# Optimization experiments

Hardware: AMD Instinct MI355X
Metric: run time of the kernel (lower is better)

## Reference

```python
import jax, jax.numpy as jnp
import numpy as np

N, F_IN, H, C, E = 50000, 128, 4, 32, 800000
NEG_SLOPE = 0.2


def setup_inputs() -> dict:
    key = jax.random.key(0)
    ks = jax.random.split(key, 6)
    x = jax.random.normal(ks[0], (N, F_IN), dtype=jnp.float32)
    edge_index = jax.random.randint(ks[1], (2, E), 0, N, dtype=jnp.int64)
    scale = 1.0 / np.sqrt(F_IN)
    Wl = jax.random.normal(ks[2], (F_IN, H * C), dtype=jnp.float32) * scale
    Wr = jax.random.normal(ks[3], (F_IN, H * C), dtype=jnp.float32) * scale
    att = jax.random.normal(ks[4], (H, C), dtype=jnp.float32) * (1.0 / np.sqrt(C))
    bias = jax.random.normal(ks[5], (H * C,), dtype=jnp.float32) * 0.01
    return {"x": x, "edge_index": edge_index, "Wl": Wl, "Wr": Wr, "att": att, "bias": bias}


def reference(x, edge_index, Wl, Wr, att, bias):
    n = x.shape[0]
    # add self loops (add_self_loops=True, edge_dim=None)
    loop = jnp.arange(n, dtype=edge_index.dtype)
    ei = jnp.concatenate([edge_index, jnp.stack([loop, loop])], axis=1)
    src, dst = ei[0], ei[1]  # messages flow src -> dst; softmax over dst
    # share_weights=False: separate projections for source (l) and target (r)
    xl = (x @ Wl).reshape(n, H, C)
    xr = (x @ Wr).reshape(n, H, C)
    # GATv2 edge score: a . LeakyReLU(xl[src] + xr[dst])
    e = xl[src] + xr[dst]                      # [Et, H, C]
    e = jnp.where(e > 0, e, NEG_SLOPE * e)
    logits = jnp.einsum('ehc,hc->eh', e, att)  # [Et, H]
    # segment softmax over destination nodes (every node has a self loop)
    m = jax.ops.segment_max(logits, dst, num_segments=n)
    ex = jnp.exp(logits - m[dst])
    den = jax.ops.segment_sum(ex, dst, num_segments=n)
    alpha = ex / den[dst]                      # [Et, H]
    # weighted scatter-aggregate of source messages
    out = jax.ops.segment_sum(alpha[:, :, None] * xl[src], dst, num_segments=n)
    out = out.reshape(n, H * C) + bias         # concat=True heads, bias
    out = jax.nn.relu(out)                     # activation_func='relu'
    return out, alpha
```

## Files before the change

kernel.cpp:

```cpp
#include <hip/hip_runtime.h>
#include <hip/hip_bf16.h>

#define F_IN   128
#define HC     128
#define NH     4
#define NEG_SLOPE 0.2f
#define CAP    5120

typedef __attribute__((ext_vector_type(8))) short short8;
typedef __attribute__((ext_vector_type(4))) float f32x4;

__device__ __forceinline__ unsigned short f2bf(float f) {
    union { float f; unsigned u; } c; c.f = f;
    unsigned u = c.u;
    u += 0x7FFFu + ((u >> 16) & 1u);
    return (unsigned short)(u >> 16);
}
__device__ __forceinline__ float bflo(unsigned u) {
    union { unsigned u; float f; } c; c.u = u << 16; return c.f;
}
__device__ __forceinline__ float bfhi(unsigned u) {
    union { unsigned u; float f; } c; c.u = u & 0xFFFF0000u; return c.f;
}

__global__ __launch_bounds__(256) void wpack_zero_kernel(
    const float* __restrict__ Wl, const float* __restrict__ Wr,
    short* __restrict__ BlP, short* __restrict__ BrP,
    int* __restrict__ bucketCount)
{
    if ((int)blockIdx.x >= 16) {
        bucketCount[threadIdx.x] = 0;
        return;
    }
    const int tid = blockIdx.x * 256 + threadIdx.x;
    const int mat = tid >> 11;
    const int r   = tid & 2047;
    const int f   = r >> 6;
    const int l   = r & 63;
    const int t   = f & 3;
    const int ct  = f >> 2;
    const int kb  = t * 32 + (l >> 4) * 8;
    const int c   = ct * 16 + (l & 15);
    const float* W = mat ? Wr : Wl;
    short*       P = mat ? BrP : BlP;
    short8 v;
    #pragma unroll
    for (int j = 0; j < 8; ++j)
        v[j] = (short)f2bf(W[(size_t)(kb + j) * HC + c]);
    *(short8*)&P[(size_t)(f * 64 + l) * 8] = v;
}

__global__ __launch_bounds__(256) void proj_split_kernel(
    const float* __restrict__ x,
    const short* __restrict__ BlP,
    const short* __restrict__ BrP,
    unsigned short* __restrict__ xlb,
    unsigned short* __restrict__ xrb,
    const int* __restrict__ ei,
    int* __restrict__ bucketCount,
    int* __restrict__ slotDst,
    int2* __restrict__ slotES,
    int n, int E, int PB, int NB)
{
    __shared__ int sA[256];
    __shared__ int sB[256];

    if ((int)blockIdx.x >= PB) {
        const int t  = threadIdx.x;
        const int e0 = ((int)blockIdx.x - PB) * 4096;

        sA[t] = 0;
        __syncthreads();
        #pragma unroll
        for (int k = 0; k < 16; ++k) {
            const int e = e0 + k * 256 + t;
            if (e < E) atomicAdd(&sA[ei[E + e] >> 8], 1);
        }
        __syncthreads();
        if (t < NB) sB[t] = atomicAdd(&bucketCount[t], sA[t]);
        __syncthreads();
        sA[t] = 0;
        __syncthreads();
        #pragma unroll
        for (int k = 0; k < 16; ++k) {
            const int e = e0 + k * 256 + t;
            if (e < E) {
                const int d = ei[E + e];
                const int b = d >> 8;
                const int r = sB[b] + atomicAdd(&sA[b], 1);
                slotDst[(size_t)b * CAP + r] = d;
                slotES [(size_t)b * CAP + r] = make_int2(e, ei[e]);
            }
        }
        return;
    }

    const int w    = threadIdx.x >> 6;
    const int lane = threadIdx.x & 63;
    const int r0   = blockIdx.x * 64 + w * 16;
    if (r0 >= n) return;
    const int q    = lane >> 4;
    const int row  = r0 + (lane & 15);

    short8 af[4];
    {
        const float* xp = x + (size_t)row * F_IN + q * 8;
        #pragma unroll
        for (int t = 0; t < 4; ++t) {
            const float4 u0 = *(const float4*)(xp + t * 32);
            const float4 u1 = *(const float4*)(xp + t * 32 + 4);
            short8 a;
            a[0] = (short)f2bf(u0.x); a[1] = (short)f2bf(u0.y);
            a[2] = (short)f2bf(u0.z); a[3] = (short)f2bf(u0.w);
            a[4] = (short)f2bf(u1.x); a[5] = (short)f2bf(u1.y);
            a[6] = (short)f2bf(u1.z); a[7] = (short)f2bf(u1.w);
            af[t] = a;
        }
    }

    f32x4 accL[8], accR[8];
    const f32x4 zero = {0.f, 0.f, 0.f, 0.f};
    #pragma unroll
    for (int ct = 0; ct < 8; ++ct) { accL[ct] = zero; accR[ct] = zero; }

    #pragma unroll
    for (int t = 0; t < 4; ++t) {
        #pragma unroll
        for (int ct = 0; ct < 8; ++ct) {
            const short8 bl = *(const short8*)&BlP[(size_t)((ct * 4 + t) * 64 + lane) * 8];
            const short8 br = *(const short8*)&BrP[(size_t)((ct * 4 + t) * 64 + lane) * 8];
            accL[ct] = __builtin_amdgcn_mfma_f32_16x16x32_bf16(af[t], bl, accL[ct], 0, 0, 0);
            accR[ct] = __builtin_amdgcn_mfma_f32_16x16x32_bf16(af[t], br, accR[ct], 0, 0, 0);
        }
    }

    const int cb = lane & 15;
    const bool evenLane = (cb & 1) == 0;
    unsigned* xl_u = (unsigned*)xlb;
    unsigned* xr_u = (unsigned*)xrb;
    #pragma unroll
    for (int ct = 0; ct < 8; ++ct) {
        #pragma unroll
        for (int i = 0; i < 4; ++i) {
            const float l = accL[ct][i];
            const float r = accR[ct][i];
            const float sl = __shfl_xor(l, 1);
            const float sr = __shfl_xor(r, 1);
            const int rowo = r0 + q * 4 + i;
            const size_t cidx = (size_t)rowo * 64 + ct * 8 + (cb >> 1);
            if (evenLane) xl_u[cidx] = (unsigned)f2bf(l)  | ((unsigned)f2bf(sl) << 16);
            else          xr_u[cidx] = (unsigned)f2bf(sr) | ((unsigned)f2bf(r)  << 16);
        }
    }
}

__global__ __launch_bounds__(256) void bucket_build_kernel(
    const int* __restrict__ bucketCount,
    const int* __restrict__ slotDst,
    const int2* __restrict__ slotES,
    int* __restrict__ rowptr,
    int2* __restrict__ csr,
    int n, int E, int NB)
{
    __shared__ int sh[256];
    __shared__ int cur[256];
    const int t = threadIdx.x;
    const int b = blockIdx.x;

    sh[t] = (t < NB) ? bucketCount[t] : 0;
    __syncthreads();
    for (int off = 1; off < 256; off <<= 1) {
        int v = sh[t]; int u = (t >= off) ? sh[t - off] : 0;
        __syncthreads();
        sh[t] = v + u;
        __syncthreads();
    }
    const int base = (b == 0) ? 0 : sh[b - 1];
    const int cnt  = sh[b] - base;
    __syncthreads();

    cur[t] = 0;
    __syncthreads();
    const size_t sbase = (size_t)b * CAP;
    for (int i = t; i < cnt; i += 256)
        atomicAdd(&cur[slotDst[sbase + i] & 255], 1);
    __syncthreads();

    const int myCnt = cur[t];
    sh[t] = myCnt;
    __syncthreads();
    for (int off = 1; off < 256; off <<= 1) {
        int v = sh[t]; int u = (t >= off) ? sh[t - off] : 0;
        __syncthreads();
        sh[t] = v + u;
        __syncthreads();
    }
    const int startT = sh[t] - myCnt;
    const int dstT = (b << 8) + t;
    if (dstT < n) rowptr[dstT] = base + startT;
    if (b == 0 && t == 0) rowptr[n] = E;
    __syncthreads();
    cur[t] = startT;
    __syncthreads();

    for (int i = t; i < cnt; i += 256) {
        const int d = slotDst[sbase + i];
        const int r = atomicAdd(&cur[d & 255], 1);
        csr[(size_t)base + r] = slotES[sbase + i];
    }
}

__global__ __launch_bounds__(256) void fused_agg_kernel(
    const int2* __restrict__ csr,
    const int* __restrict__ rowptr,
    const unsigned short* __restrict__ xlb,
    const unsigned short* __restrict__ xrb,
    const float* __restrict__ att,
    const float* __restrict__ bias,
    float* __restrict__ alpha_out,
    float* __restrict__ out,
    int n, int E)
{
    __shared__ float lds_ex[4][256];
    const int w    = threadIdx.x >> 6;
    const int lane = threadIdx.x & 63;
    const int dst  = blockIdx.x * 4 + w;
    if (dst >= n) return;

    const int start = rowptr[dst];
    const int deg   = rowptr[dst + 1] - start;
    const int total = deg + 1;
    const int g     = lane >> 4;
    const int i     = lane & 15;
    const int h     = i >> 2;

    const uint4* xl_u = (const uint4*)xlb;

    float xrv[8], attv[8];
    {
        const uint4 ur = ((const uint4*)xrb)[(size_t)dst * 16 + i];
        xrv[0] = bflo(ur.x); xrv[1] = bfhi(ur.x);
        xrv[2] = bflo(ur.y); xrv[3] = bfhi(ur.y);
        xrv[4] = bflo(ur.z); xrv[5] = bfhi(ur.z);
        xrv[6] = bflo(ur.w); xrv[7] = bfhi(ur.w);
        const float4 a01 = *(const float4*)&att[8 * i];
        const float4 a23 = *(const float4*)&att[8 * i + 4];
        attv[0] = a01.x; attv[1] = a01.y; attv[2] = a01.z; attv[3] = a01.w;
        attv[4] = a23.x; attv[5] = a23.y; attv[6] = a23.z; attv[7] = a23.w;
    }

    int eReg = E + dst, srcReg = dst;
    if (lane < deg) { const int2 es = csr[start + lane]; eReg = es.x; srcReg = es.y; }

    float* exrow = lds_ex[w];

    float dh = 0.f;
    float acc[8];
    #pragma unroll
    for (int k = 0; k < 8; ++k) acc[k] = 0.f;

    int j = 0;
    {
        const int s0 = __shfl(srcReg, g);
        uint4 u = xl_u[(size_t)s0 * 16 + i];
        uint4 u1 = u;
        if (4 < total) {
            const int s1 = __shfl(srcReg, min(g + 4, 63));
            u1 = xl_u[(size_t)s1 * 16 + i];
        }

        for (; j < total && j <= 60; j += 4) {
            const int jj = j + g;
            uint4 u2 = u1;
            if (j + 8 < total) {
                const int sn = __shfl(srcReg, min(jj + 8, 63));
                u2 = xl_u[(size_t)sn * 16 + i];
            }

            float v[8];
            v[0] = bflo(u.x); v[1] = bfhi(u.x);
            v[2] = bflo(u.y); v[3] = bfhi(u.y);
            v[4] = bflo(u.z); v[5] = bfhi(u.z);
            v[6] = bflo(u.w); v[7] = bfhi(u.w);

            float p = 0.f;
            #pragma unroll
            for (int k = 0; k < 8; ++k) {
                float t = v[k] + xrv[k];
                t = fmaxf(t, NEG_SLOPE * t);
                p = fmaf(attv[k], t, p);
            }
            p += __shfl_xor(p, 1);
            p += __shfl_xor(p, 2);

            const float ex = (jj <= deg) ? __expf(p) : 0.f;
            dh += ex;
            #pragma unroll
            for (int k = 0; k < 8; ++k) acc[k] = fmaf(ex, v[k], acc[k]);

            if ((lane & 3) == 0 && jj <= deg) exrow[jj * 4 + h] = ex;
            u = u1; u1 = u2;
        }
    }
    for (; j < total; j += 4) {
        const int jj = j + g;
        const int cidx = start + min(jj, deg - 1);
        const int2 es = csr[cidx];
        const int s   = (jj < deg) ? es.y : dst;
        const int eId = (jj < deg) ? es.x : E + dst;
        const uint4 u = xl_u[(size_t)s * 16 + i];

        float v[8];
        v[0] = bflo(u.x); v[1] = bfhi(u.x);
        v[2] = bflo(u.y); v[3] = bfhi(u.y);
        v[4] = bflo(u.z); v[5] = bfhi(u.z);
        v[6] = bflo(u.w); v[7] = bfhi(u.w);

        float p = 0.f;
        #pragma unroll
        for (int k = 0; k < 8; ++k) {
            float t = v[k] + xrv[k];
            t = fmaxf(t, NEG_SLOPE * t);
            p = fmaf(attv[k], t, p);
        }
        p += __shfl_xor(p, 1);
        p += __shfl_xor(p, 2);

        const float ex = (jj <= deg) ? __expf(p) : 0.f;
        dh += ex;
        #pragma unroll
        for (int k = 0; k < 8; ++k) acc[k] = fmaf(ex, v[k], acc[k]);

        if ((lane & 3) == 0 && jj <= deg) alpha_out[(size_t)eId * NH + h] = ex;
    }

    dh += __shfl_xor(dh, 16);
    dh += __shfl_xor(dh, 32);
    #pragma unroll
    for (int k = 0; k < 8; ++k) {
        acc[k] += __shfl_xor(acc[k], 16);
        acc[k] += __shfl_xor(acc[k], 32);
    }
    const float invh = 1.f / dh;
    const float id0 = 1.f / __shfl(dh, 0);
    const float id1 = 1.f / __shfl(dh, 4);
    const float id2 = 1.f / __shfl(dh, 8);
    const float id3 = 1.f / __shfl(dh, 12);

    __threadfence_block();

    if (lane < total && lane < 64) {
        const float4 e4 = *(const float4*)&exrow[lane * 4];
        const float4 a4 = make_float4(e4.x * id0, e4.y * id1, e4.z * id2, e4.w * id3);
        *(float4*)&alpha_out[(size_t)eReg * NH] = a4;
    }
    if (total > 64) {
        __threadfence();
        for (int jr = 64 + lane; jr < total; jr += 64) {
            const int e = (jr < deg) ? csr[start + jr].x : E + dst;
            float4 a4 = *(float4*)&alpha_out[(size_t)e * NH];
            a4.x *= id0; a4.y *= id1; a4.z *= id2; a4.w *= id3;
            *(float4*)&alpha_out[(size_t)e * NH] = a4;
        }
    }

    if (g == 0) {
        const float4 b01 = *(const float4*)&bias[8 * i];
        const float4 b23 = *(const float4*)&bias[8 * i + 4];
        float4 o01, o23;
        o01.x = fmaxf(fmaf(acc[0], invh, b01.x), 0.f);
        o01.y = fmaxf(fmaf(acc[1], invh, b01.y), 0.f);
        o01.z = fmaxf(fmaf(acc[2], invh, b01.z), 0.f);
        o01.w = fmaxf(fmaf(acc[3], invh, b01.w), 0.f);
        o23.x = fmaxf(fmaf(acc[4], invh, b23.x), 0.f);
        o23.y = fmaxf(fmaf(acc[5], invh, b23.y), 0.f);
        o23.z = fmaxf(fmaf(acc[6], invh, b23.z), 0.f);
        o23.w = fmaxf(fmaf(acc[7], invh, b23.w), 0.f);
        *(float4*)&out[(size_t)dst * HC + 8 * i]     = o01;
        *(float4*)&out[(size_t)dst * HC + 8 * i + 4] = o23;
    }
}

extern "C" void kernel_launch(void* const* d_in, const int* in_sizes, int n_in,
                              void* d_out, int out_size, void* d_ws, size_t ws_size,
                              hipStream_t stream)
{
    const float* x    = (const float*)d_in[0];
    const int*   ei   = (const int*)d_in[1];
    const float* Wl   = (const float*)d_in[2];
    const float* Wr   = (const float*)d_in[3];
    const float* att  = (const float*)d_in[4];
    const float* bias = (const float*)d_in[5];

    const int n  = in_sizes[0] / F_IN;
    const int E  = in_sizes[1] / 2;
    const int NB = (n + 255) >> 8;

    float* out   = (float*)d_out;
    float* alpha = (float*)d_out + (size_t)n * HC;

    short*          BlP         = (short*)d_ws;
    short*          BrP         = BlP + 16384;
    unsigned short* xlb         = (unsigned short*)(BrP + 16384);
    unsigned short* xrb         = xlb + (size_t)n * HC;
    int2*           csr         = (int2*)(xrb + (size_t)n * HC);
    int2*           slotES      = csr + E;
    int*            slotDst     = (int*)(slotES + (size_t)NB * CAP);
    int*            bucketCount = slotDst + (size_t)NB * CAP;
    int*            rowptr      = bucketCount + 256;

    const int PB = (n + 63) / 64;
    const int SB = (E + 4095) / 4096;

    wpack_zero_kernel<<<dim3(17), 256, 0, stream>>>(Wl, Wr, BlP, BrP, bucketCount);

    proj_split_kernel<<<dim3(PB + SB), 256, 0, stream>>>(
        x, BlP, BrP, xlb, xrb, ei, bucketCount, slotDst, slotES, n, E, PB, NB);

    bucket_build_kernel<<<dim3(NB), 256, 0, stream>>>(
        bucketCount, slotDst, slotES, rowptr, csr, n, E, NB);

    fused_agg_kernel<<<dim3((n + 3) / 4), 256, 0, stream>>>(
        csr, rowptr, xlb, xrb, att, bias, alpha, out, n, E);
}
```

Measured before the change: 181.4 us.

## Switch features to fp16 with packed dot2, pack dst into edge ids, enlarge blocks

Projected features are now stored as fp16 instead of bf16, so the aggregation kernel can do the add, LeakyReLU and attention dot product with packed half2 math and fdot2. The separate slotDst array is dropped by packing the low 8 bits of dst into the top byte of the edge id. The bucket build now reads each slot record once into registers. The projection, split and bucket kernels move to 1024-thread blocks. This trades precision and range behaviour (fp16 overflow, fp16 attention weights) for less memory traffic and fewer ALU ops, and it assumes edge ids fit in 24 bits and at most 5 records per thread.

```diff
diff --git a/kernel.cpp b/kernel.cpp
--- a/kernel.cpp
+++ b/kernel.cpp
@@ -1,5 +1,6 @@
 #include <hip/hip_runtime.h>
 #include <hip/hip_bf16.h>
+#include <hip/hip_fp16.h>
 
 #define F_IN   128
 #define HC     128
@@ -9,6 +10,7 @@
 
 typedef __attribute__((ext_vector_type(8))) short short8;
 typedef __attribute__((ext_vector_type(4))) float f32x4;
+typedef _Float16 h2 __attribute__((ext_vector_type(2)));
 
 __device__ __forceinline__ unsigned short f2bf(float f) {
     union { float f; unsigned u; } c; c.f = f;
@@ -16,12 +18,16 @@
     u += 0x7FFFu + ((u >> 16) & 1u);
     return (unsigned short)(u >> 16);
 }
-__device__ __forceinline__ float bflo(unsigned u) {
-    union { unsigned u; float f; } c; c.u = u << 16; return c.f;
-}
-__device__ __forceinline__ float bfhi(unsigned u) {
-    union { unsigned u; float f; } c; c.u = u & 0xFFFF0000u; return c.f;
-}
+
+__device__ __forceinline__ float fdot2f(h2 a, h2 b, float c) {
+#if __has_builtin(__builtin_amdgcn_fdot2)
+    return __builtin_amdgcn_fdot2(a, b, c, false);
+#else
+    return fmaf((float)a[0], (float)b[0], fmaf((float)a[1], (float)b[1], c));
+#endif
+}
+
+union U4H { uint4 u; h2 h[4]; };
 
 __global__ __launch_bounds__(256) void wpack_zero_kernel(
     const float* __restrict__ Wl, const float* __restrict__ Wr,
@@ -50,7 +56,7 @@
     *(short8*)&P[(size_t)(f * 64 + l) * 8] = v;
 }
 
-__global__ __launch_bounds__(256) void proj_split_kernel(
+__global__ __launch_bounds__(1024) void proj_split_kernel(
     const float* __restrict__ x,
     const short* __restrict__ BlP,
     const short* __restrict__ BrP,
@@ -58,46 +64,49 @@
     unsigned short* __restrict__ xrb,
     const int* __restrict__ ei,
     int* __restrict__ bucketCount,
-    int* __restrict__ slotDst,
     int2* __restrict__ slotES,
     int n, int E, int PB, int NB)
 {
     __shared__ int sA[256];
     __shared__ int sB[256];
+    const int t = threadIdx.x;
 
     if ((int)blockIdx.x >= PB) {
-        const int t  = threadIdx.x;
         const int e0 = ((int)blockIdx.x - PB) * 4096;
 
-        sA[t] = 0;
-        __syncthreads();
-        #pragma unroll
-        for (int k = 0; k < 16; ++k) {
-            const int e = e0 + k * 256 + t;
-            if (e < E) atomicAdd(&sA[ei[E + e] >> 8], 1);
-        }
+        if (t < 256) sA[t] = 0;
+        __syncthreads();
+        int dsts[4], srcs[4];
+        #pragma unroll
+        for (int k = 0; k < 4; ++k) {
+            const int e = e0 + k * 1024 + t;
+            dsts[k] = (e < E) ? ei[E + e] : -1;
+            srcs[k] = (e < E) ? ei[e] : 0;
+        }
+        #pragma unroll
+        for (int k = 0; k < 4; ++k)
+            if (dsts[k] >= 0) atomicAdd(&sA[dsts[k] >> 8], 1);
         __syncthreads();
         if (t < NB) sB[t] = atomicAdd(&bucketCount[t], sA[t]);
         __syncthreads();
-        sA[t] = 0;
-        __syncthreads();
-        #pragma unroll
-        for (int k = 0; k < 16; ++k) {
-            const int e = e0 + k * 256 + t;
-            if (e < E) {
-                const int d = ei[E + e];
-                const int b = d >> 8;
+        if (t < 256) sA[t] = 0;
+        __syncthreads();
+        #pragma unroll
+        for (int k = 0; k < 4; ++k) {
+            const int e = e0 + k * 1024 + t;
+            if (dsts[k] >= 0) {
+                const int b = dsts[k] >> 8;
                 const int r = sB[b] + atomicAdd(&sA[b], 1);
-                slotDst[(size_t)b * CAP + r] = d;
-                slotES [(size_t)b * CAP + r] = make_int2(e, ei[e]);
+                slotES[(size_t)b * CAP + r] =
+                    make_int2(e | ((dsts[k] & 255) << 24), srcs[k]);
             }
         }
         return;
     }
 
-    const int w    = threadIdx.x >> 6;
-    const int lane = threadIdx.x & 63;
-    const int r0   = blockIdx.x * 64 + w * 16;
+    const int w    = t >> 6;
+    const int lane = t & 63;
+    const int r0   = blockIdx.x * 256 + w * 16;
     if (r0 >= n) return;
     const int q    = lane >> 4;
     const int row  = r0 + (lane & 15);
@@ -106,15 +115,15 @@
     {
         const float* xp = x + (size_t)row * F_IN + q * 8;
         #pragma unroll
-        for (int t = 0; t < 4; ++t) {
-            const float4 u0 = *(const float4*)(xp + t * 32);
-            const float4 u1 = *(const float4*)(xp + t * 32 + 4);
+        for (int s = 0; s < 4; ++s) {
+            const float4 u0 = *(const float4*)(xp + s * 32);
+            const float4 u1 = *(const float4*)(xp + s * 32 + 4);
             short8 a;
             a[0] = (short)f2bf(u0.x); a[1] = (short)f2bf(u0.y);
             a[2] = (short)f2bf(u0.z); a[3] = (short)f2bf(u0.w);
             a[4] = (short)f2bf(u1.x); a[5] = (short)f2bf(u1.y);
             a[6] = (short)f2bf(u1.z); a[7] = (short)f2bf(u1.w);
-            af[t] = a;
+            af[s] = a;
         }
     }
 
@@ -124,13 +133,13 @@
     for (int ct = 0; ct < 8; ++ct) { accL[ct] = zero; accR[ct] = zero; }
 
     #pragma unroll
-    for (int t = 0; t < 4; ++t) {
+    for (int s = 0; s < 4; ++s) {
         #pragma unroll
         for (int ct = 0; ct < 8; ++ct) {
-            const short8 bl = *(const short8*)&BlP[(size_t)((ct * 4 + t) * 64 + lane) * 8];
-            const short8 br = *(const short8*)&BrP[(size_t)((ct * 4 + t) * 64 + lane) * 8];
-            accL[ct] = __builtin_amdgcn_mfma_f32_16x16x32_bf16(af[t], bl, accL[ct], 0, 0, 0);
-            accR[ct] = __builtin_amdgcn_mfma_f32_16x16x32_bf16(af[t], br, accR[ct], 0, 0, 0);
+            const short8 bl = *(const short8*)&BlP[(size_t)((ct * 4 + s) * 64 + lane) * 8];
+            const short8 br = *(const short8*)&BrP[(size_t)((ct * 4 + s) * 64 + lane) * 8];
+            accL[ct] = __builtin_amdgcn_mfma_f32_16x16x32_bf16(af[s], bl, accL[ct], 0, 0, 0);
+            accR[ct] = __builtin_amdgcn_mfma_f32_16x16x32_bf16(af[s], br, accR[ct], 0, 0, 0);
         }
     }
 
@@ -148,15 +157,15 @@
             const float sr = __shfl_xor(r, 1);
             const int rowo = r0 + q * 4 + i;
             const size_t cidx = (size_t)rowo * 64 + ct * 8 + (cb >> 1);
-            if (evenLane) xl_u[cidx] = (unsigned)f2bf(l)  | ((unsigned)f2bf(sl) << 16);
-            else          xr_u[cidx] = (unsigned)f2bf(sr) | ((unsigned)f2bf(r)  << 16);
-        }
-    }
-}
-
-__global__ __launch_bounds__(256) void bucket_build_kernel(
+            union { _Float16 h[2]; unsigned u; } ph;
+            if (evenLane) { ph.h[0] = (_Float16)l;  ph.h[1] = (_Float16)sl; xl_u[cidx] = ph.u; }
+            else          { ph.h[0] = (_Float16)sr; ph.h[1] = (_Float16)r;  xr_u[cidx] = ph.u; }
+        }
+    }
+}
+
+__global__ __launch_bounds__(1024) void bucket_build_kernel(
     const int* __restrict__ bucketCount,
-    const int* __restrict__ slotDst,
     const int2* __restrict__ slotES,
     int* __restrict__ rowptr,
     int2* __restrict__ csr,
@@ -167,46 +176,54 @@
     const int t = threadIdx.x;
     const int b = blockIdx.x;
 
-    sh[t] = (t < NB) ? bucketCount[t] : 0;
+    if (t < 256) sh[t] = (t < NB) ? bucketCount[t] : 0;
     __syncthreads();
     for (int off = 1; off < 256; off <<= 1) {
-        int v = sh[t]; int u = (t >= off) ? sh[t - off] : 0;
-        __syncthreads();
-        sh[t] = v + u;
+        int v = 0, u = 0;
+        if (t < 256) { v = sh[t]; u = (t >= off) ? sh[t - off] : 0; }
+        __syncthreads();
+        if (t < 256) sh[t] = v + u;
         __syncthreads();
     }
     const int base = (b == 0) ? 0 : sh[b - 1];
     const int cnt  = sh[b] - base;
     __syncthreads();
 
-    cur[t] = 0;
+    if (t < 256) cur[t] = 0;
     __syncthreads();
     const size_t sbase = (size_t)b * CAP;
-    for (int i = t; i < cnt; i += 256)
-        atomicAdd(&cur[slotDst[sbase + i] & 255], 1);
-    __syncthreads();
-
-    const int myCnt = cur[t];
-    sh[t] = myCnt;
+    int2 rec[5]; int nrec = 0;
+    for (int i = t; i < cnt; i += 1024) {
+        rec[nrec] = slotES[sbase + i];
+        ++nrec;
+    }
+    for (int k = 0; k < nrec; ++k)
+        atomicAdd(&cur[(unsigned)rec[k].x >> 24], 1);
+    __syncthreads();
+
+    int myCnt = 0;
+    if (t < 256) { myCnt = cur[t]; sh[t] = myCnt; }
     __syncthreads();
     for (int off = 1; off < 256; off <<= 1) {
-        int v = sh[t]; int u = (t >= off) ? sh[t - off] : 0;
-        __syncthreads();
-        sh[t] = v + u;
-        __syncthreads();
-    }
-    const int startT = sh[t] - myCnt;
-    const int dstT = (b << 8) + t;
-    if (dstT < n) rowptr[dstT] = base + startT;
-    if (b == 0 && t == 0) rowptr[n] = E;
-    __syncthreads();
-    cur[t] = startT;
-    __syncthreads();
-
-    for (int i = t; i < cnt; i += 256) {
-        const int d = slotDst[sbase + i];
-        const int r = atomicAdd(&cur[d & 255], 1);
-        csr[(size_t)base + r] = slotES[sbase + i];
+        int v = 0, u = 0;
+        if (t < 256) { v = sh[t]; u = (t >= off) ? sh[t - off] : 0; }
+        __syncthreads();
+        if (t < 256) sh[t] = v + u;
+        __syncthreads();
+    }
+    if (t < 256) {
+        const int startT = sh[t] - myCnt;
+        const int dstT = (b << 8) + t;
+        if (dstT < n) rowptr[dstT] = base + startT;
+        if (b == 0 && t == 0) rowptr[n] = E;
+        cur[t] = startT;
+    }
+    __syncthreads();
+
+    for (int k = 0; k < nrec; ++k) {
+        const int dl = (unsigned)rec[k].x >> 24;
+        const int r = atomicAdd(&cur[dl], 1);
+        csr[(size_t)base + r] = make_int2(rec[k].x & 0xFFFFFF, rec[k].y);
     }
 }
 
@@ -236,18 +253,18 @@
 
     const uint4* xl_u = (const uint4*)xlb;
 
-    float xrv[8], attv[8];
+    h2 xr2[4], at2[4];
     {
-        const uint4 ur = ((const uint4*)xrb)[(size_t)dst * 16 + i];
-        xrv[0] = bflo(ur.x); xrv[1] = bfhi(ur.x);
-        xrv[2] = bflo(ur.y); xrv[3] = bfhi(ur.y);
-        xrv[4] = bflo(ur.z); xrv[5] = bfhi(ur.z);
-        xrv[6] = bflo(ur.w); xrv[7] = bfhi(ur.w);
+        U4H c; c.u = ((const uint4*)xrb)[(size_t)dst * 16 + i];
+        xr2[0] = c.h[0]; xr2[1] = c.h[1]; xr2[2] = c.h[2]; xr2[3] = c.h[3];
         const float4 a01 = *(const float4*)&att[8 * i];
         const float4 a23 = *(const float4*)&att[8 * i + 4];
-        attv[0] = a01.x; attv[1] = a01.y; attv[2] = a01.z; attv[3] = a01.w;
-        attv[4] = a23.x; attv[5] = a23.y; attv[6] = a23.z; attv[7] = a23.w;
-    }
+        at2[0] = h2{(_Float16)a01.x, (_Float16)a01.y};
+        at2[1] = h2{(_Float16)a01.z, (_Float16)a01.w};
+        at2[2] = h2{(_Float16)a23.x, (_Float16)a23.y};
+        at2[3] = h2{(_Float16)a23.z, (_Float16)a23.w};
+    }
+    const h2 slope2 = {(_Float16)NEG_SLOPE, (_Float16)NEG_SLOPE};
 
     int eReg = E + dst, srcReg = dst;
     if (lane < deg) { const int2 es = csr[start + lane]; eReg = es.x; srcReg = es.y; }
@@ -277,18 +294,17 @@
                 u2 = xl_u[(size_t)sn * 16 + i];
             }
 
-            float v[8];
-            v[0] = bflo(u.x); v[1] = bfhi(u.x);
-            v[2] = bflo(u.y); v[3] = bfhi(u.y);
-            v[4] = bflo(u.z); v[5] = bfhi(u.z);
-            v[6] = bflo(u.w); v[7] = bfhi(u.w);
-
+            U4H cu; cu.u = u;
             float p = 0.f;
+            float vf[8];
             #pragma unroll
-            for (int k = 0; k < 8; ++k) {
-                float t = v[k] + xrv[k];
-                t = fmaxf(t, NEG_SLOPE * t);
-                p = fmaf(attv[k], t, p);
+            for (int k = 0; k < 4; ++k) {
+                const h2 v2 = cu.h[k];
+                const h2 t2 = v2 + xr2[k];
+                const h2 l2 = __builtin_elementwise_max(t2, t2 * slope2);
+                p = fdot2f(l2, at2[k], p);
+                vf[2 * k]     = (float)v2[0];
+                vf[2 * k + 1] = (float)v2[1];
             }
             p += __shfl_xor(p, 1);
             p += __shfl_xor(p, 2);
@@ -296,7 +312,7 @@
             const float ex = (jj <= deg) ? __expf(p) : 0.f;
             dh += ex;
             #pragma unroll
-            for (int k = 0; k < 8; ++k) acc[k] = fmaf(ex, v[k], acc[k]);
+            for (int k = 0; k < 8; ++k) acc[k] = fmaf(ex, vf[k], acc[k]);
 
             if ((lane & 3) == 0 && jj <= deg) exrow[jj * 4 + h] = ex;
             u = u1; u1 = u2;
@@ -308,20 +324,18 @@
         const int2 es = csr[cidx];
         const int s   = (jj < deg) ? es.y : dst;
         const int eId = (jj < deg) ? es.x : E + dst;
-        const uint4 u = xl_u[(size_t)s * 16 + i];
-
-        float v[8];
-        v[0] = bflo(u.x); v[1] = bfhi(u.x);
-        v[2] = bflo(u.y); v[3] = bfhi(u.y);
-        v[4] = bflo(u.z); v[5] = bfhi(u.z);
-        v[6] = bflo(u.w); v[7] = bfhi(u.w);
+        U4H cu; cu.u = xl_u[(size_t)s * 16 + i];
 
         float p = 0.f;
-        #pragma unroll
-        for (int k = 0; k < 8; ++k) {
-            float t = v[k] + xrv[k];
-            t = fmaxf(t, NEG_SLOPE * t);
-            p = fmaf(attv[k], t, p);
+        float vf[8];
+        #pragma unroll
+        for (int k = 0; k < 4; ++k) {
+            const h2 v2 = cu.h[k];
+            const h2 t2 = v2 + xr2[k];
+            const h2 l2 = __builtin_elementwise_max(t2, t2 * slope2);
+            p = fdot2f(l2, at2[k], p);
+            vf[2 * k]     = (float)v2[0];
+            vf[2 * k + 1] = (float)v2[1];
         }
         p += __shfl_xor(p, 1);
         p += __shfl_xor(p, 2);
@@ -329,7 +343,7 @@
         const float ex = (jj <= deg) ? __expf(p) : 0.f;
         dh += ex;
         #pragma unroll
-        for (int k = 0; k < 8; ++k) acc[k] = fmaf(ex, v[k], acc[k]);
+        for (int k = 0; k < 8; ++k) acc[k] = fmaf(ex, vf[k], acc[k]);
 
         if ((lane & 3) == 0 && jj <= deg) alpha_out[(size_t)eId * NH + h] = ex;
     }
@@ -405,20 +419,19 @@
     unsigned short* xrb         = xlb + (size_t)n * HC;
     int2*           csr         = (int2*)(xrb + (size_t)n * HC);
     int2*           slotES      = csr + E;
-    int*            slotDst     = (int*)(slotES + (size_t)NB * CAP);
-    int*            bucketCount = slotDst + (size_t)NB * CAP;
+    int*            bucketCount = (int*)(slotES + (size_t)NB * CAP);
     int*            rowptr      = bucketCount + 256;
 
-    const int PB = (n + 63) / 64;
+    const int PB = (n + 255) / 256;
     const int SB = (E + 4095) / 4096;
 
     wpack_zero_kernel<<<dim3(17), 256, 0, stream>>>(Wl, Wr, BlP, BrP, bucketCount);
 
-    proj_split_kernel<<<dim3(PB + SB), 256, 0, stream>>>(
-        x, BlP, BrP, xlb, xrb, ei, bucketCount, slotDst, slotES, n, E, PB, NB);
-
-    bucket_build_kernel<<<dim3(NB), 256, 0, stream>>>(
-        bucketCount, slotDst, slotES, rowptr, csr, n, E, NB);
+    proj_split_kernel<<<dim3(PB + SB), 1024, 0, stream>>>(
+        x, BlP, BrP, xlb, xrb, ei, bucketCount, slotES, n, E, PB, NB);
+
+    bucket_build_kernel<<<dim3(NB), 1024, 0, stream>>>(
+        bucketCount, slotES, rowptr, csr, n, E, NB);
 
     fused_agg_kernel<<<dim3((n + 3) / 4), 256, 0, stream>>>(
         csr, rowptr, xlb, xrb, att, bias, alpha, out, n, E);
```

New measurement: 174.9 us. -3.6%, faster.
